# Optimization experiments

Measured on AMD Instinct MI355X. Metric: run time of the kernel, lower is better.

## Reference

```python
import jax, jax.numpy as jnp
import numpy as np
from jax import lax

STRIDE = (1, 1)
PADDING = ((1, 1), (1, 1))
DILATION = (1, 1)


def setup_inputs() -> dict:
    key = jax.random.key(0)
    k1, k2 = jax.random.split(key)
    input = jax.random.normal(k1, (32, 128, 56, 56), dtype=jnp.float32)
    weight = jax.random.normal(k2, (256, 128, 3, 3), dtype=jnp.float32)
    bias = jnp.zeros((256,), dtype=jnp.float32)
    return {"input": input, "weight": weight, "bias": bias}


def reference(input, weight, bias):
    # The original builds the conv's dense matrix via conv2d on an identity
    # basis and then matmuls; that is mathematically identical to a direct
    # conv2d (the map is linear), plus the broadcast bias.
    out = lax.conv_general_dilated(
        input, weight,
        window_strides=STRIDE,
        padding=PADDING,
        rhs_dilation=DILATION,
        dimension_numbers=("NCHW", "OIHW", "NCHW"),
    )
    return out + bias[None, :, None, None]
```

## Files before the change

kernel.cpp:

```cpp
#include <hip/hip_runtime.h>
#include <hip/hip_bf16.h>
#include <stdint.h>


typedef __attribute__((ext_vector_type(8))) short bf16x8;
typedef __attribute__((ext_vector_type(8))) unsigned short ushort8;
typedef __attribute__((ext_vector_type(4))) float f32x4;

#define HW       56
#define SPATIAL  3136
#define C_IN     128
#define K_OUT    256
#define GEMM_K   1152
#define GEMM_N   100352

#define PHW      58
#define PIMG     3364
#define PADTOT_AL 107656

#define NTILE    18
#define BUFH     16384

__device__ __forceinline__ unsigned short f2bf(float f) {
    union { float f; unsigned int u; } v; v.f = f;
    unsigned int u = v.u + 0x7FFFu + ((v.u >> 16) & 1u);
    return (unsigned short)(u >> 16);
}

__device__ __forceinline__ void gload16(const unsigned short* g, unsigned short* l) {
    __builtin_amdgcn_global_load_lds(
        (const __attribute__((address_space(1))) unsigned int*)(g),
        (__attribute__((address_space(3))) unsigned int*)(l),
        16, 0, 0);
}

__global__ __launch_bounds__(256)
void prep_kernel(const float* __restrict__ w, unsigned short* __restrict__ w3,
                 unsigned short* __restrict__ pad) {
    if (blockIdx.x < 1152) {
        int idx = blockIdx.x * 256 + threadIdx.x;
        int rc   = idx / 18432;
        int rem  = idx % 18432;
        int tap  = rem / 2048;
        int rem2 = rem % 2048;
        int cc   = rem2 / 512;
        int s    = rem2 % 512;
        int l    = s >> 3, j = s & 7;
        int ko   = rc * 16 + (l & 15);
        int c    = cc * 32 + ((l >> 4) << 3) + j;
        w3[idx] = f2bf(w[(ko * C_IN + c) * 9 + tap]);
    } else {
        int idx = (blockIdx.x - 1152) * 256 + threadIdx.x;
        if (idx >= 29184) return;
        int cc  = idx / 7296;
        int r   = idx % 7296;
        int img = r / 228;
        int p   = r % 228;
        int pos;
        if (p < 58)       pos = p;
        else if (p < 116) pos = 57 * PHW + (p - 58);
        else { int i = p - 116; pos = (1 + (i >> 1)) * PHW + (i & 1) * 57; }
        unsigned short* d = pad + (size_t)cc * PADTOT_AL * 32
                          + ((size_t)img * PIMG + pos) * 32;
        const ushort8 z = (ushort8){0,0,0,0,0,0,0,0};
        *reinterpret_cast<ushort8*>(d)      = z;
        *reinterpret_cast<ushort8*>(d + 8)  = z;
        *reinterpret_cast<ushort8*>(d + 16) = z;
        *reinterpret_cast<ushort8*>(d + 24) = z;
    }
}

__global__ __launch_bounds__(256)
void intrans_kernel(const float* __restrict__ in, unsigned short* __restrict__ pad) {
    __shared__ __attribute__((aligned(16))) unsigned short l[56 * 136];
    const int bx = blockIdx.x;
    const int n = bx / HW, h = bx % HW;
    const int tid = threadIdx.x;
    const float* src = in + (size_t)n * C_IN * SPATIAL + h * HW;
    #pragma unroll
    for (int i = 0; i < 28; ++i) {
        int idx = i * 256 + tid;
        int c = idx / HW, w = idx % HW;
        l[w * 136 + c] = f2bf(src[(size_t)c * SPATIAL + w]);
    }
    __syncthreads();
    const int prow = n * PIMG + (h + 1) * PHW;
    #pragma unroll
    for (int j = 0; j < 4; ++j) {
        int chunk = j * 256 + tid;
        if (chunk < 896) {
            int w = chunk >> 4, c8 = chunk & 15;
            int cc = c8 >> 2, sub = c8 & 3;
            unsigned short* dst = pad + (size_t)cc * PADTOT_AL * 32
                                + (size_t)(prow + w + 1) * 32 + sub * 8;
            *reinterpret_cast<ushort8*>(dst) =
                *reinterpret_cast<const ushort8*>(&l[w * 136 + c8 * 8]);
        }
    }
}

__global__ __launch_bounds__(256, 2)
void conv_kd(const unsigned short* __restrict__ pad,
             const unsigned short* __restrict__ w3,
             const float* __restrict__ bias,
             float* __restrict__ out) {
    __shared__ __attribute__((aligned(16))) unsigned short lds[2 * BUFH];

    const int tid  = threadIdx.x;
    const int wave = tid >> 6;
    const int lane = tid & 63;
    const int la   = lane & 15;
    const int lkh  = lane >> 4;

    const int bid = blockIdx.x;
    const int swz = (bid & 7) * 196 + (bid >> 3);
    const int mt  = swz & 1, nt = swz >> 1;
    const int m0  = mt * 128;
    const int g0  = nt * 128;

    const int wr = wave >> 1, wc = wave & 1;

    const unsigned short* aw0 = w3 + (size_t)(mt * 8 + wave * 2 + 0) * 18432 + lane * 8;
    const unsigned short* aw1 = w3 + (size_t)(mt * 8 + wave * 2 + 1) * 18432 + lane * 8;
    const unsigned short* bsrc0;
    const unsigned short* bsrc1;
    {
        int col = g0 + (wave * 2 + 0) * 16 + la;
        int img = col / SPATIAL;
        int pos = col - img * SPATIAL;
        int oh  = pos / HW, ow = pos - oh * HW;
        bsrc0 = pad + (size_t)(img * PIMG + (oh + 1) * PHW + (ow + 1)) * 32 + lkh * 8;
        col = g0 + (wave * 2 + 1) * 16 + la;
        img = col / SPATIAL;
        pos = col - img * SPATIAL;
        oh  = pos / HW; ow = pos - oh * HW;
        bsrc1 = pad + (size_t)(img * PIMG + (oh + 1) * PHW + (ow + 1)) * 32 + lkh * 8;
    }

    f32x4 acc[4][4];
    #pragma unroll
    for (int i = 0; i < 4; ++i)
        #pragma unroll
        for (int j = 0; j < 4; ++j)
            acc[i][j] = (f32x4){0.f, 0.f, 0.f, 0.f};

    auto STAGE = [&](int tn, int kc) {
        const int tap = tn >> 1;
        const int cc  = (tn & 1) * 2 + kc;
        const int dr = tap / 3 - 1, dsx = tap % 3 - 1;
        unsigned short* dst = &lds[(tn & 1) * BUFH];
        const ptrdiff_t bofs = (ptrdiff_t)cc * (PADTOT_AL * 32) + (dr * PHW + dsx) * 32;
        gload16(aw0 + (size_t)(tap * 4 + cc) * 512, dst + ((wave * 2 + 0) * 2 + kc) * 512);
        gload16(aw1 + (size_t)(tap * 4 + cc) * 512, dst + ((wave * 2 + 1) * 2 + kc) * 512);
        gload16(bsrc0 + bofs, dst + 8192 + ((wave * 2 + 0) * 2 + kc) * 512);
        gload16(bsrc1 + bofs, dst + 8192 + ((wave * 2 + 1) * 2 + kc) * 512);
    };

    bf16x8 af0[4], af1[4], bv0[4], bv1[4];

    STAGE(0, 0); STAGE(0, 1); STAGE(1, 0);
    asm volatile("s_waitcnt vmcnt(4)" ::: "memory");
    __builtin_amdgcn_s_barrier();

    #pragma unroll
    for (int t = 0; t < NTILE; ++t) {
        const unsigned short* Ab = &lds[(t & 1) * BUFH];

        #pragma unroll
        for (int mi = 0; mi < 4; ++mi)
            af0[mi] = *reinterpret_cast<const bf16x8*>(
                &Ab[((wr * 4 + mi) * 2 + 0) * 512 + lane * 8]);
        #pragma unroll
        for (int nj = 0; nj < 4; ++nj)
            bv0[nj] = *reinterpret_cast<const bf16x8*>(
                &Ab[8192 + ((wc * 4 + nj) * 2 + 0) * 512 + lane * 8]);
        #pragma unroll
        for (int mi = 0; mi < 4; ++mi)
            af1[mi] = *reinterpret_cast<const bf16x8*>(
                &Ab[((wr * 4 + mi) * 2 + 1) * 512 + lane * 8]);

        asm volatile("s_waitcnt lgkmcnt(4)" ::: "memory");
        __builtin_amdgcn_sched_barrier(0);
        __builtin_amdgcn_s_setprio(1);
        #pragma unroll
        for (int mi = 0; mi < 4; ++mi)
            #pragma unroll
            for (int nj = 0; nj < 4; ++nj)
                acc[mi][nj] = __builtin_amdgcn_mfma_f32_16x16x32_bf16(
                    af0[mi], bv0[nj], acc[mi][nj], 0, 0, 0);
        __builtin_amdgcn_s_setprio(0);

        __builtin_amdgcn_s_barrier();

        #pragma unroll
        for (int nj = 0; nj < 4; ++nj)
            bv1[nj] = *reinterpret_cast<const bf16x8*>(
                &Ab[8192 + ((wc * 4 + nj) * 2 + 1) * 512 + lane * 8]);
        if (t + 1 < NTILE) STAGE(t + 1, 1);
        if (t + 2 < NTILE) STAGE(t + 2, 0);

        asm volatile("s_waitcnt lgkmcnt(0)" ::: "memory");
        __builtin_amdgcn_sched_barrier(0);
        __builtin_amdgcn_s_setprio(1);
        #pragma unroll
        for (int mi = 0; mi < 4; ++mi)
            #pragma unroll
            for (int nj = 0; nj < 4; ++nj)
                acc[mi][nj] = __builtin_amdgcn_mfma_f32_16x16x32_bf16(
                    af1[mi], bv1[nj], acc[mi][nj], 0, 0, 0);
        __builtin_amdgcn_s_setprio(0);

        if (t < NTILE - 2) {
            asm volatile("s_waitcnt vmcnt(4)" ::: "memory");
            __builtin_amdgcn_s_barrier();
        } else if (t == NTILE - 2) {
            asm volatile("s_waitcnt vmcnt(0)" ::: "memory");
            __builtin_amdgcn_s_barrier();
        }
    }

    #pragma unroll
    for (int mi = 0; mi < 4; ++mi) {
        const int mb = m0 + wr * 64 + mi * 16 + lkh * 4;
        const f32x4 bv4 = *reinterpret_cast<const f32x4*>(&bias[mb]);
        #pragma unroll
        for (int nj = 0; nj < 4; ++nj) {
            const int gcol = g0 + wc * 64 + nj * 16;
            const int n2 = gcol / SPATIAL;
            const int p2 = gcol - n2 * SPATIAL + la;
            float* op = out + ((size_t)(n2 * K_OUT + mb)) * SPATIAL + p2;
            op[0]                   = acc[mi][nj][0] + bv4[0];
            op[SPATIAL]             = acc[mi][nj][1] + bv4[1];
            op[2 * SPATIAL]         = acc[mi][nj][2] + bv4[2];
            op[3 * (size_t)SPATIAL] = acc[mi][nj][3] + bv4[3];
        }
    }
}

#define LDK 40
__global__ __launch_bounds__(256)
void conv_mfma_fallback(const float* __restrict__ in,
                        const float* __restrict__ wraw,
                        const float* __restrict__ bias,
                        float* __restrict__ out) {
    __shared__ __attribute__((aligned(16))) unsigned short lA[128 * LDK];
    __shared__ __attribute__((aligned(16))) unsigned short lB[128 * LDK];
    const int tid = threadIdx.x;
    const int m0  = blockIdx.y * 128;
    const int g0  = blockIdx.x * 128;
    const int wave = tid >> 6, lane = tid & 63;
    const int wr = wave >> 1, wc = wave & 1;
    const int la = lane & 15, lkh = lane >> 4, lk = lkh * 8;

    f32x4 acc[4][4];
    #pragma unroll
    for (int i = 0; i < 4; ++i)
        #pragma unroll
        for (int j = 0; j < 4; ++j)
            acc[i][j] = (f32x4){0.f, 0.f, 0.f, 0.f};

    const int jj = tid & 127;
    const int kb = (tid >> 7) * 16;
    const int g = g0 + jj;
    const int nimg = g / SPATIAL;
    const int pos  = g % SPATIAL;
    const int oh = pos / HW, ow = pos % HW;

    for (int tap = 0; tap < 9; ++tap) {
        const int dr = tap / 3 - 1, dsx = tap % 3 - 1;
        const int ih = oh + dr, iw = ow + dsx;
        const bool valid = ((unsigned)ih < HW) && ((unsigned)iw < HW);
        const float* src = in + ((nimg * C_IN) * HW + ih) * HW + iw;
        for (int c0 = 0; c0 < C_IN; c0 += 32) {
            #pragma unroll
            for (int i = 0; i < 2; ++i) {
                const int ch = tid * 2 + i;
                const int row = ch >> 2;
                const int kp = (ch & 3) * 8;
                ushort8 v;
                #pragma unroll
                for (int e = 0; e < 8; ++e)
                    v[e] = f2bf(wraw[((m0 + row) * C_IN + c0 + kp + e) * 9 + tap]);
                *reinterpret_cast<ushort8*>(&lA[row * LDK + kp]) = v;
            }
            {
                ushort8 v0, v1;
                #pragma unroll
                for (int i = 0; i < 8; ++i)
                    v0[i] = f2bf(valid ? src[(c0 + kb + i) * SPATIAL] : 0.f);
                #pragma unroll
                for (int i = 0; i < 8; ++i)
                    v1[i] = f2bf(valid ? src[(c0 + kb + 8 + i) * SPATIAL] : 0.f);
                *reinterpret_cast<ushort8*>(&lB[jj * LDK + kb])     = v0;
                *reinterpret_cast<ushort8*>(&lB[jj * LDK + kb + 8]) = v1;
            }
            __syncthreads();
            bf16x8 af[4], bv[4];
            #pragma unroll
            for (int f = 0; f < 4; ++f) {
                af[f] = *reinterpret_cast<const bf16x8*>(&lA[(wr * 64 + f * 16 + la) * LDK + lk]);
                bv[f] = *reinterpret_cast<const bf16x8*>(&lB[(wc * 64 + f * 16 + la) * LDK + lk]);
            }
            #pragma unroll
            for (int fi = 0; fi < 4; ++fi)
                #pragma unroll
                for (int fj = 0; fj < 4; ++fj)
                    acc[fi][fj] = __builtin_amdgcn_mfma_f32_16x16x32_bf16(
                        af[fi], bv[fj], acc[fi][fj], 0, 0, 0);
            __syncthreads();
        }
    }
    const int mbase = m0 + wr * 64;
    const int cbase = g0 + wc * 64;
    #pragma unroll
    for (int fi = 0; fi < 4; ++fi) {
        float bvv[4];
        #pragma unroll
        for (int r = 0; r < 4; ++r)
            bvv[r] = bias[mbase + fi * 16 + lkh * 4 + r];
        #pragma unroll
        for (int fj = 0; fj < 4; ++fj) {
            const int gcol = cbase + fj * 16 + la;
            const int n2 = gcol / SPATIAL;
            const int p2 = gcol % SPATIAL;
            float* op = out + (size_t)(n2 * K_OUT) * SPATIAL + p2;
            #pragma unroll
            for (int r = 0; r < 4; ++r)
                op[(size_t)(mbase + fi * 16 + lkh * 4 + r) * SPATIAL] = acc[fi][fj][r] + bvv[r];
        }
    }
}

extern "C" void kernel_launch(void* const* d_in, const int* in_sizes, int n_in,
                              void* d_out, int out_size, void* d_ws, size_t ws_size,
                              hipStream_t stream) {
    const float* in   = (const float*)d_in[0];
    const float* w    = (const float*)d_in[1];
    const float* bias = (const float*)d_in[2];
    float* out = (float*)d_out;

    const size_t pad_halves = 4ull * PADTOT_AL * 32ull;
    const size_t need_bytes = (pad_halves + 294912ull) * 2ull;

    if (ws_size >= need_bytes) {
        unsigned short* pad = (unsigned short*)d_ws;
        unsigned short* w3  = pad + pad_halves;
        prep_kernel<<<1152 + 114, 256, 0, stream>>>(w, w3, pad);
        intrans_kernel<<<32 * HW, 256, 0, stream>>>(in, pad);
        conv_kd<<<(GEMM_N / 128) * (K_OUT / 128), 256, 0, stream>>>(pad, w3, bias, out);
    } else {
        dim3 grid(GEMM_N / 128, K_OUT / 128);
        conv_mfma_fallback<<<grid, 256, 0, stream>>>(in, w, bias, out);
    }
}
```

Baseline: 99.47 us.

## Load weight fragments directly to registers and triple-buffer activation tiles in LDS

The A (weight) operand is no longer staged through LDS. Each wave loads its weight fragments straight from global memory into registers, double-buffered across even and odd tiles. The B (activation) tile now goes through a three-slot LDS ring, prefetched two tiles ahead, with one barrier per tile instead of two. This cuts LDS traffic and synchronisation, but adds register pressure from 16 extra A vectors and exposes global load latency for the weights.

Result: slower. 105.7 us (+6.3%).

```diff
diff --git a/kernel.cpp b/kernel.cpp
--- a/kernel.cpp
+++ b/kernel.cpp
@@ -19,7 +19,7 @@
 #define PADTOT_AL 107656
 
 #define NTILE    18
-#define BUFH     16384
+#define BBUF     8192
 
 __device__ __forceinline__ unsigned short f2bf(float f) {
     union { float f; unsigned int u; } v; v.f = f;
@@ -100,11 +100,11 @@
 }
 
 __global__ __launch_bounds__(256, 2)
-void conv_kd(const unsigned short* __restrict__ pad,
-             const unsigned short* __restrict__ w3,
-             const float* __restrict__ bias,
-             float* __restrict__ out) {
-    __shared__ __attribute__((aligned(16))) unsigned short lds[2 * BUFH];
+void conv_hyb(const unsigned short* __restrict__ pad,
+              const unsigned short* __restrict__ w3,
+              const float* __restrict__ bias,
+              float* __restrict__ out) {
+    __shared__ __attribute__((aligned(16))) unsigned short lds[3 * BBUF];
 
     const int tid  = threadIdx.x;
     const int wave = tid >> 6;
@@ -120,8 +120,11 @@
 
     const int wr = wave >> 1, wc = wave & 1;
 
-    const unsigned short* aw0 = w3 + (size_t)(mt * 8 + wave * 2 + 0) * 18432 + lane * 8;
-    const unsigned short* aw1 = w3 + (size_t)(mt * 8 + wave * 2 + 1) * 18432 + lane * 8;
+    const unsigned short* asrc[4];
+    #pragma unroll
+    for (int mi = 0; mi < 4; ++mi)
+        asrc[mi] = w3 + (size_t)(mt * 8 + wr * 4 + mi) * 18432 + lane * 8;
+
     const unsigned short* bsrc0;
     const unsigned short* bsrc1;
     {
@@ -144,79 +147,93 @@
         for (int j = 0; j < 4; ++j)
             acc[i][j] = (f32x4){0.f, 0.f, 0.f, 0.f};
 
-    auto STAGE = [&](int tn, int kc) {
+    auto STAGEB = [&](int tn) {
         const int tap = tn >> 1;
-        const int cc  = (tn & 1) * 2 + kc;
         const int dr = tap / 3 - 1, dsx = tap % 3 - 1;
-        unsigned short* dst = &lds[(tn & 1) * BUFH];
-        const ptrdiff_t bofs = (ptrdiff_t)cc * (PADTOT_AL * 32) + (dr * PHW + dsx) * 32;
-        gload16(aw0 + (size_t)(tap * 4 + cc) * 512, dst + ((wave * 2 + 0) * 2 + kc) * 512);
-        gload16(aw1 + (size_t)(tap * 4 + cc) * 512, dst + ((wave * 2 + 1) * 2 + kc) * 512);
-        gload16(bsrc0 + bofs, dst + 8192 + ((wave * 2 + 0) * 2 + kc) * 512);
-        gload16(bsrc1 + bofs, dst + 8192 + ((wave * 2 + 1) * 2 + kc) * 512);
+        unsigned short* dst = &lds[(tn % 3) * BBUF];
+        #pragma unroll
+        for (int kc = 0; kc < 2; ++kc) {
+            const int cc = (tn & 1) * 2 + kc;
+            const ptrdiff_t bofs = (ptrdiff_t)cc * (PADTOT_AL * 32)
+                                 + (dr * PHW + dsx) * 32;
+            gload16(bsrc0 + bofs, dst + (((wave * 2 + 0) * 2) + kc) * 512);
+            gload16(bsrc1 + bofs, dst + (((wave * 2 + 1) * 2) + kc) * 512);
+        }
     };
 
-    bf16x8 af0[4], af1[4], bv0[4], bv1[4];
-
-    STAGE(0, 0); STAGE(0, 1); STAGE(1, 0);
-    asm volatile("s_waitcnt vmcnt(4)" ::: "memory");
-    __builtin_amdgcn_s_barrier();
+    bf16x8 aE[8], aO[8], bv0[4], bv1[4];
+
+#define LOADA(tn, A_) do {                                                   \
+    const int tap_ = (tn) >> 1;                                              \
+    _Pragma("unroll")                                                        \
+    for (int ks = 0; ks < 2; ++ks) {                                         \
+        const int cc_ = ((tn) & 1) * 2 + ks;                                 \
+        const ptrdiff_t ao_ = (ptrdiff_t)(tap_ * 4 + cc_) * 512;             \
+        _Pragma("unroll")                                                    \
+        for (int mi = 0; mi < 4; ++mi)                                       \
+            A_[mi * 2 + ks] = *reinterpret_cast<const bf16x8*>(asrc[mi] + ao_); \
+    }                                                                        \
+} while (0)
+
+    LOADA(0, aE);
+    STAGEB(0); STAGEB(1); STAGEB(2);
 
     #pragma unroll
     for (int t = 0; t < NTILE; ++t) {
-        const unsigned short* Ab = &lds[(t & 1) * BUFH];
-
-        #pragma unroll
-        for (int mi = 0; mi < 4; ++mi)
-            af0[mi] = *reinterpret_cast<const bf16x8*>(
-                &Ab[((wr * 4 + mi) * 2 + 0) * 512 + lane * 8]);
+        if (t == 0)                asm volatile("s_waitcnt vmcnt(8)" ::: "memory");
+        else if (t <= NTILE - 3)   asm volatile("s_waitcnt vmcnt(4)" ::: "memory");
+        else                       asm volatile("s_waitcnt vmcnt(0)" ::: "memory");
+        __builtin_amdgcn_s_barrier();
+
+        const unsigned short* Bb = &lds[(t % 3) * BBUF];
         #pragma unroll
         for (int nj = 0; nj < 4; ++nj)
             bv0[nj] = *reinterpret_cast<const bf16x8*>(
-                &Ab[8192 + ((wc * 4 + nj) * 2 + 0) * 512 + lane * 8]);
-        #pragma unroll
-        for (int mi = 0; mi < 4; ++mi)
-            af1[mi] = *reinterpret_cast<const bf16x8*>(
-                &Ab[((wr * 4 + mi) * 2 + 1) * 512 + lane * 8]);
+                &Bb[((wc * 4 + nj) * 2 + 0) * 512 + lane * 8]);
+        #pragma unroll
+        for (int nj = 0; nj < 4; ++nj)
+            bv1[nj] = *reinterpret_cast<const bf16x8*>(
+                &Bb[((wc * 4 + nj) * 2 + 1) * 512 + lane * 8]);
+
+        if ((t & 1) == 0) { if (t + 1 < NTILE) LOADA(t + 1, aO); }
+        else              { if (t + 1 < NTILE) LOADA(t + 1, aE); }
+        if (t + 2 < NTILE) STAGEB(t + 2);
 
         asm volatile("s_waitcnt lgkmcnt(4)" ::: "memory");
         __builtin_amdgcn_sched_barrier(0);
         __builtin_amdgcn_s_setprio(1);
-        #pragma unroll
-        for (int mi = 0; mi < 4; ++mi)
-            #pragma unroll
-            for (int nj = 0; nj < 4; ++nj)
-                acc[mi][nj] = __builtin_amdgcn_mfma_f32_16x16x32_bf16(
-                    af0[mi], bv0[nj], acc[mi][nj], 0, 0, 0);
+        if ((t & 1) == 0) {
+            #pragma unroll
+            for (int mi = 0; mi < 4; ++mi)
+                #pragma unroll
+                for (int nj = 0; nj < 4; ++nj)
+                    acc[mi][nj] = __builtin_amdgcn_mfma_f32_16x16x32_bf16(
+                        aE[mi * 2 + 0], bv0[nj], acc[mi][nj], 0, 0, 0);
+            asm volatile("s_waitcnt lgkmcnt(0)" ::: "memory");
+            __builtin_amdgcn_sched_barrier(0);
+            #pragma unroll
+            for (int mi = 0; mi < 4; ++mi)
+                #pragma unroll
+                for (int nj = 0; nj < 4; ++nj)
+                    acc[mi][nj] = __builtin_amdgcn_mfma_f32_16x16x32_bf16(
+                        aE[mi * 2 + 1], bv1[nj], acc[mi][nj], 0, 0, 0);
+        } else {
+            #pragma unroll
+            for (int mi = 0; mi < 4; ++mi)
+                #pragma unroll
+                for (int nj = 0; nj < 4; ++nj)
+                    acc[mi][nj] = __builtin_amdgcn_mfma_f32_16x16x32_bf16(
+                        aO[mi * 2 + 0], bv0[nj], acc[mi][nj], 0, 0, 0);
+            asm volatile("s_waitcnt lgkmcnt(0)" ::: "memory");
+            __builtin_amdgcn_sched_barrier(0);
+            #pragma unroll
+            for (int mi = 0; mi < 4; ++mi)
+                #pragma unroll
+                for (int nj = 0; nj < 4; ++nj)
+                    acc[mi][nj] = __builtin_amdgcn_mfma_f32_16x16x32_bf16(
+                        aO[mi * 2 + 1], bv1[nj], acc[mi][nj], 0, 0, 0);
+        }
         __builtin_amdgcn_s_setprio(0);
-
-        __builtin_amdgcn_s_barrier();
-
-        #pragma unroll
-        for (int nj = 0; nj < 4; ++nj)
-            bv1[nj] = *reinterpret_cast<const bf16x8*>(
-                &Ab[8192 + ((wc * 4 + nj) * 2 + 1) * 512 + lane * 8]);
-        if (t + 1 < NTILE) STAGE(t + 1, 1);
-        if (t + 2 < NTILE) STAGE(t + 2, 0);
-
-        asm volatile("s_waitcnt lgkmcnt(0)" ::: "memory");
-        __builtin_amdgcn_sched_barrier(0);
-        __builtin_amdgcn_s_setprio(1);
-        #pragma unroll
-        for (int mi = 0; mi < 4; ++mi)
-            #pragma unroll
-            for (int nj = 0; nj < 4; ++nj)
-                acc[mi][nj] = __builtin_amdgcn_mfma_f32_16x16x32_bf16(
-                    af1[mi], bv1[nj], acc[mi][nj], 0, 0, 0);
-        __builtin_amdgcn_s_setprio(0);
-
-        if (t < NTILE - 2) {
-            asm volatile("s_waitcnt vmcnt(4)" ::: "memory");
-            __builtin_amdgcn_s_barrier();
-        } else if (t == NTILE - 2) {
-            asm volatile("s_waitcnt vmcnt(0)" ::: "memory");
-            __builtin_amdgcn_s_barrier();
-        }
     }
 
     #pragma unroll
@@ -235,6 +252,7 @@
             op[3 * (size_t)SPATIAL] = acc[mi][nj][3] + bv4[3];
         }
     }
+#undef LOADA
 }
 
 #define LDK 40
@@ -347,7 +365,7 @@
         unsigned short* w3  = pad + pad_halves;
         prep_kernel<<<1152 + 114, 256, 0, stream>>>(w, w3, pad);
         intrans_kernel<<<32 * HW, 256, 0, stream>>>(in, pad);
-        conv_kd<<<(GEMM_N / 128) * (K_OUT / 128), 256, 0, stream>>>(pad, w3, bias, out);
+        conv_hyb<<<(GEMM_N / 128) * (K_OUT / 128), 256, 0, stream>>>(pad, w3, bias, out);
     } else {
         dim3 grid(GEMM_N / 128, K_OUT / 128);
         conv_mfma_fallback<<<grid, 256, 0, stream>>>(in, w, bias, out);
```

## Enlarge conv GEMM tile to 256x256 with 16-wave 1024-thread blocks

Applied to the files above, without the earlier changes.

Replaces the 128x128 tile, 4-wave block GEMM with a 256x256 tile computed by 16 waves (1024 threads), covering all 256 output channels in one block. Each wave now stages one A and one B chunk per k-step, and the LDS double buffer doubles to 128 KB. The larger tile halves global/L2 traffic per FLOP, since each input column is loaded once instead of once per M-tile. In exchange it runs one block per CU with 392 blocks, which can leave tail imbalance across CUs and gives less latency hiding between blocks.

Result: no change. 98.86 us (-0.6%).

```diff
diff --git a/kernel.cpp b/kernel.cpp
--- a/kernel.cpp
+++ b/kernel.cpp
@@ -18,8 +18,10 @@
 #define PIMG     3364
 #define PADTOT_AL 107656
 
+#define BM       256
+#define BN       256
 #define NTILE    18
-#define BUFH     16384
+#define BUFH     32768
 
 __device__ __forceinline__ unsigned short f2bf(float f) {
     union { float f; unsigned int u; } v; v.f = f;
@@ -99,11 +101,11 @@
     }
 }
 
-__global__ __launch_bounds__(256, 2)
-void conv_kd(const unsigned short* __restrict__ pad,
-             const unsigned short* __restrict__ w3,
-             const float* __restrict__ bias,
-             float* __restrict__ out) {
+__global__ __launch_bounds__(1024, 1)
+void conv_tlp2(const unsigned short* __restrict__ pad,
+               const unsigned short* __restrict__ w3,
+               const float* __restrict__ bias,
+               float* __restrict__ out) {
     __shared__ __attribute__((aligned(16))) unsigned short lds[2 * BUFH];
 
     const int tid  = threadIdx.x;
@@ -113,28 +115,19 @@
     const int lkh  = lane >> 4;
 
     const int bid = blockIdx.x;
-    const int swz = (bid & 7) * 196 + (bid >> 3);
-    const int mt  = swz & 1, nt = swz >> 1;
-    const int m0  = mt * 128;
-    const int g0  = nt * 128;
-
-    const int wr = wave >> 1, wc = wave & 1;
-
-    const unsigned short* aw0 = w3 + (size_t)(mt * 8 + wave * 2 + 0) * 18432 + lane * 8;
-    const unsigned short* aw1 = w3 + (size_t)(mt * 8 + wave * 2 + 1) * 18432 + lane * 8;
-    const unsigned short* bsrc0;
-    const unsigned short* bsrc1;
+    const int nt  = (bid & 7) * 49 + (bid >> 3);
+    const int g0  = nt * BN;
+
+    const int wr = wave >> 2, wc = wave & 3;
+
+    const unsigned short* aw = w3 + (size_t)wave * 18432 + lane * 8;
+    const unsigned short* bsrc;
     {
-        int col = g0 + (wave * 2 + 0) * 16 + la;
+        int col = g0 + wave * 16 + la;
         int img = col / SPATIAL;
         int pos = col - img * SPATIAL;
         int oh  = pos / HW, ow = pos - oh * HW;
-        bsrc0 = pad + (size_t)(img * PIMG + (oh + 1) * PHW + (ow + 1)) * 32 + lkh * 8;
-        col = g0 + (wave * 2 + 1) * 16 + la;
-        img = col / SPATIAL;
-        pos = col - img * SPATIAL;
-        oh  = pos / HW; ow = pos - oh * HW;
-        bsrc1 = pad + (size_t)(img * PIMG + (oh + 1) * PHW + (ow + 1)) * 32 + lkh * 8;
+        bsrc = pad + (size_t)(img * PIMG + (oh + 1) * PHW + (ow + 1)) * 32 + lkh * 8;
     }
 
     f32x4 acc[4][4];
@@ -149,17 +142,15 @@
         const int cc  = (tn & 1) * 2 + kc;
         const int dr = tap / 3 - 1, dsx = tap % 3 - 1;
         unsigned short* dst = &lds[(tn & 1) * BUFH];
-        const ptrdiff_t bofs = (ptrdiff_t)cc * (PADTOT_AL * 32) + (dr * PHW + dsx) * 32;
-        gload16(aw0 + (size_t)(tap * 4 + cc) * 512, dst + ((wave * 2 + 0) * 2 + kc) * 512);
-        gload16(aw1 + (size_t)(tap * 4 + cc) * 512, dst + ((wave * 2 + 1) * 2 + kc) * 512);
-        gload16(bsrc0 + bofs, dst + 8192 + ((wave * 2 + 0) * 2 + kc) * 512);
-        gload16(bsrc1 + bofs, dst + 8192 + ((wave * 2 + 1) * 2 + kc) * 512);
+        gload16(aw + (size_t)(tap * 4 + cc) * 512, dst + (wave * 2 + kc) * 512);
+        gload16(bsrc + (size_t)cc * (PADTOT_AL * 32) + (dr * PHW + dsx) * 32,
+                dst + 16384 + (wave * 2 + kc) * 512);
     };
 
     bf16x8 af0[4], af1[4], bv0[4], bv1[4];
 
     STAGE(0, 0); STAGE(0, 1); STAGE(1, 0);
-    asm volatile("s_waitcnt vmcnt(4)" ::: "memory");
+    asm volatile("s_waitcnt vmcnt(2)" ::: "memory");
     __builtin_amdgcn_s_barrier();
 
     #pragma unroll
@@ -173,7 +164,7 @@
         #pragma unroll
         for (int nj = 0; nj < 4; ++nj)
             bv0[nj] = *reinterpret_cast<const bf16x8*>(
-                &Ab[8192 + ((wc * 4 + nj) * 2 + 0) * 512 + lane * 8]);
+                &Ab[16384 + ((wc * 4 + nj) * 2 + 0) * 512 + lane * 8]);
         #pragma unroll
         for (int mi = 0; mi < 4; ++mi)
             af1[mi] = *reinterpret_cast<const bf16x8*>(
@@ -195,7 +186,7 @@
         #pragma unroll
         for (int nj = 0; nj < 4; ++nj)
             bv1[nj] = *reinterpret_cast<const bf16x8*>(
-                &Ab[8192 + ((wc * 4 + nj) * 2 + 1) * 512 + lane * 8]);
+                &Ab[16384 + ((wc * 4 + nj) * 2 + 1) * 512 + lane * 8]);
         if (t + 1 < NTILE) STAGE(t + 1, 1);
         if (t + 2 < NTILE) STAGE(t + 2, 0);
 
@@ -211,7 +202,7 @@
         __builtin_amdgcn_s_setprio(0);
 
         if (t < NTILE - 2) {
-            asm volatile("s_waitcnt vmcnt(4)" ::: "memory");
+            asm volatile("s_waitcnt vmcnt(2)" ::: "memory");
             __builtin_amdgcn_s_barrier();
         } else if (t == NTILE - 2) {
             asm volatile("s_waitcnt vmcnt(0)" ::: "memory");
@@ -221,7 +212,7 @@
 
     #pragma unroll
     for (int mi = 0; mi < 4; ++mi) {
-        const int mb = m0 + wr * 64 + mi * 16 + lkh * 4;
+        const int mb = wr * 64 + mi * 16 + lkh * 4;
         const f32x4 bv4 = *reinterpret_cast<const f32x4*>(&bias[mb]);
         #pragma unroll
         for (int nj = 0; nj < 4; ++nj) {
@@ -347,7 +338,7 @@
         unsigned short* w3  = pad + pad_halves;
         prep_kernel<<<1152 + 114, 256, 0, stream>>>(w, w3, pad);
         intrans_kernel<<<32 * HW, 256, 0, stream>>>(in, pad);
-        conv_kd<<<(GEMM_N / 128) * (K_OUT / 128), 256, 0, stream>>>(pad, w3, bias, out);
+        conv_tlp2<<<GEMM_N / BN, 1024, 0, stream>>>(pad, w3, bias, out);
     } else {
         dim3 grid(GEMM_N / 128, K_OUT / 128);
         conv_mfma_fallback<<<grid, 256, 0, stream>>>(in, w, bias, out);
```
